# Performance work log

Measured on AMD Instinct MI355X. Metric: run time of the kernel, lower is better.

## Reference

```python
import jax, jax.numpy as jnp
from jax import lax
import numpy as np

VOCAB_SIZE = 510
N_LABELS = VOCAB_SIZE + 2  # 512; start_idx = N_LABELS-2, stop_idx = N_LABELS-1
BATCH = 128
SEQ_LEN = 256
NEG_INF = -10000.0  # matches torch fill value (finite, not -inf)


def setup_inputs() -> dict:
    key = jax.random.key(0)
    k_logits, k_lens, k_trans = jax.random.split(key, 3)
    logits = jax.random.normal(k_logits, (BATCH, SEQ_LEN, N_LABELS), dtype=jnp.float32)
    # lengths in [1, SEQ_LEN] so every sequence has at least one real step
    lens = jax.random.randint(k_lens, (BATCH,), 1, SEQ_LEN + 1, dtype=jnp.int64)
    # learned parameter: transitions[i, j] = score of transitioning j -> i
    transitions = jax.random.normal(k_trans, (N_LABELS, N_LABELS), dtype=jnp.float32)
    return {"logits": logits, "lens": lens, "transitions": transitions}


def reference(logits, lens, transitions):
    """CRF forward algorithm (log partition function). Returns norm: [batch]."""
    B, S, L = logits.shape
    start_idx = L - 2
    stop_idx = L - 1

    alpha0 = jnp.full((B, L), NEG_INF, dtype=logits.dtype).at[:, start_idx].set(0.0)

    def step(carry, logit_t):
        alpha, rem = carry  # alpha: [B, L], rem: [B]
        # scores[b, i, j] = transitions[i, j] + alpha[b, j] + logit_t[b, i]
        scores = transitions[None, :, :] + alpha[:, None, :] + logit_t[:, :, None]
        alpha_next = jax.nn.logsumexp(scores, axis=2)  # [B, L]
        mask = (rem > 0)[:, None]
        alpha = jnp.where(mask, alpha_next, alpha)
        return (alpha, rem - 1), None

    logits_t = jnp.swapaxes(logits, 0, 1)  # [S, B, L]
    (alpha, _), _ = lax.scan(step, (alpha0, lens), logits_t)

    alpha = alpha + transitions[stop_idx][None, :]
    norm = jax.nn.logsumexp(alpha, axis=1)  # [B]
    return norm
```

## Files before the change

kernel.cpp:

```cpp
#include <hip/hip_runtime.h>


typedef _Float16 h2 __attribute__((ext_vector_type(2)));

#define NB 128
#define NS 256
#define NL 512

#define SMEM_ELDS_BYTES (NL * 16 * 16)
#define SMEM_Y_OFF      SMEM_ELDS_BYTES
#define SMEM_RED_OFF    (SMEM_ELDS_BYTES + NL * 2)
#define SMEM_TOTAL      (SMEM_RED_OFF + 64)

__device__ __forceinline__ float dot2acc(unsigned int e, unsigned int y, float acc) {
#if __has_builtin(__builtin_amdgcn_fdot2)
    return __builtin_amdgcn_fdot2(__builtin_bit_cast(h2, e),
                                  __builtin_bit_cast(h2, y), acc, false);
#else
    h2 eh = __builtin_bit_cast(h2, e);
    h2 yh = __builtin_bit_cast(h2, y);
    return acc + (float)eh[0] * (float)yh[0] + (float)eh[1] * (float)yh[1];
#endif
}

__device__ __forceinline__ unsigned int pk2(float a, float b) {
    h2 h;
    h[0] = (_Float16)a;
    h[1] = (_Float16)b;
    return __builtin_bit_cast(unsigned int, h);
}

__global__ __launch_bounds__(512, 2) void crf_fwd_kernel(
    const float* __restrict__ logits,
    const int*   __restrict__ lens_raw,
    const float* __restrict__ trans,
    float* __restrict__ out)
{
    extern __shared__ char smem[];
    uint4*          e_lds = (uint4*)smem;
    unsigned short* y_sh  = (unsigned short*)(smem + SMEM_Y_OFF);
    float*          red   = (float*)(smem + SMEM_RED_OFF);

    const int b    = blockIdx.x;
    const int i    = threadIdx.x;
    const int lane = i & 63;
    const int wid  = i >> 6;
    const int swz  = i & 15;

    int len;
    {
        int s1 = lens_raw[1];
        len = (s1 == 0) ? lens_raw[2 * b] : lens_raw[b];
        len = min(max(len, 0), NS);
    }

    const float4* trow4 = (const float4*)(trans + (size_t)i * NL);

    float m = -3.4e38f;
    for (int c = 0; c < NL / 4; ++c) {
        float4 v = trow4[c];
        m = fmaxf(m, fmaxf(fmaxf(v.x, v.y), fmaxf(v.z, v.w)));
    }
    #pragma unroll
    for (int off = 32; off; off >>= 1) m = fmaxf(m, __shfl_xor(m, off));
    if (lane == 0) red[wid] = m;
    __syncthreads();
    float T = red[0];
    #pragma unroll
    for (int k = 1; k < 8; ++k) T = fmaxf(T, red[k]);
    __syncthreads();

    unsigned int Ereg[192];
    #pragma unroll
    for (int c = 0; c < 96; ++c) {
        float4 v = trow4[c];
        Ereg[2 * c]     = pk2(__expf(v.x - T), __expf(v.y - T));
        Ereg[2 * c + 1] = pk2(__expf(v.z - T), __expf(v.w - T));
    }
    #pragma unroll
    for (int c = 0; c < 16; ++c) {
        float4 a = trow4[96 + 2 * c];
        float4 d = trow4[97 + 2 * c];
        uint4 w;
        w.x = pk2(__expf(a.x - T), __expf(a.y - T));
        w.y = pk2(__expf(a.z - T), __expf(a.w - T));
        w.z = pk2(__expf(d.x - T), __expf(d.y - T));
        w.w = pk2(__expf(d.z - T), __expf(d.w - T));
        e_lds[i * 16 + (c ^ swz)] = w;
    }

    y_sh[i] = (i == NL - 2) ? (unsigned short)0x3C00u : (unsigned short)0u;
    float r = 0.0f;
    const float* lrow = logits + (size_t)b * NS * NL + i;
    __syncthreads();

    const uint4* y4   = (const uint4*)y_sh;
    const uint4* my_e = e_lds + i * 16;

    for (int t = 0; t < len; ++t) {
        float lg = lrow[(size_t)t * NL];
        float s0 = 0.f, s1 = 0.f, s2 = 0.f, s3 = 0.f;
        #pragma unroll
        for (int c = 0; c < 48; ++c) {
            uint4 yw = y4[c];
            s0 = dot2acc(Ereg[4 * c + 0], yw.x, s0);
            s1 = dot2acc(Ereg[4 * c + 1], yw.y, s1);
            s2 = dot2acc(Ereg[4 * c + 2], yw.z, s2);
            s3 = dot2acc(Ereg[4 * c + 3], yw.w, s3);
        }
        #pragma unroll
        for (int c = 0; c < 16; ++c) {
            uint4 ew = my_e[c ^ swz];
            uint4 yw = y4[48 + c];
            s0 = dot2acc(ew.x, yw.x, s0);
            s1 = dot2acc(ew.y, yw.y, s1);
            s2 = dot2acc(ew.z, yw.z, s2);
            s3 = dot2acc(ew.w, yw.w, s3);
        }
        float v = ((s0 + s1) + (s2 + s3)) * __expf(lg);

        float mv = v;
        #pragma unroll
        for (int off = 32; off; off >>= 1) mv = fmaxf(mv, __shfl_xor(mv, off));
        if (lane == 0) red[wid] = mv;
        __syncthreads();
        float cmax = red[0];
        #pragma unroll
        for (int k = 1; k < 8; ++k) cmax = fmaxf(cmax, red[k]);

        float yn = v * (1.0f / cmax);
        y_sh[i] = __builtin_bit_cast(unsigned short, (_Float16)yn);
        r += T + __logf(cmax);
        __syncthreads();
    }

    float yi;
    {
        _Float16 h = __builtin_bit_cast(_Float16, y_sh[i]);
        yi = (float)h;
    }
    float term = yi * __expf(trans[(size_t)(NL - 1) * NL + i] - T);
    #pragma unroll
    for (int off = 32; off; off >>= 1) term += __shfl_xor(term, off);
    if (lane == 0) red[wid] = term;
    __syncthreads();
    if (i == 0) {
        float tot = 0.f;
        #pragma unroll
        for (int k = 0; k < 8; ++k) tot += red[k];
        out[b] = r + T + __logf(tot);
    }
}

extern "C" void kernel_launch(void* const* d_in, const int* in_sizes, int n_in,
                              void* d_out, int out_size, void* d_ws, size_t ws_size,
                              hipStream_t stream) {
    const float* logits = (const float*)d_in[0];
    const int*   lens   = (const int*)d_in[1];
    const float* trans  = (const float*)d_in[2];
    float*       out    = (float*)d_out;

    hipFuncSetAttribute(reinterpret_cast<const void*>(crf_fwd_kernel),
                        hipFuncAttributeMaxDynamicSharedMemorySize, SMEM_TOTAL);

    crf_fwd_kernel<<<dim3(NB), dim3(512), SMEM_TOTAL, stream>>>(logits, lens, trans, out);
}
```

Before: 731.7 us.

## Split each transition row across two threads and hold exp-transitions fully in registers

Each label row is now handled by two threads of a 1024-thread block, each keeping 256 fp16 exp-transition values in 32 uint4 registers, so the LDS-resident portion of the matrix is dropped. The two partial dot products are combined with a lane shuffle. The logit for the next step is prefetched ahead of the recurrence. The goal is to halve the serial dot-product work per thread on each timestep and remove LDS traffic for transitions, at the cost of more waves per block and a 16-wave max reduction per step.

```diff
diff --git a/kernel.cpp b/kernel.cpp
--- a/kernel.cpp
+++ b/kernel.cpp
@@ -6,11 +6,6 @@
 #define NB 128
 #define NS 256
 #define NL 512
-
-#define SMEM_ELDS_BYTES (NL * 16 * 16)
-#define SMEM_Y_OFF      SMEM_ELDS_BYTES
-#define SMEM_RED_OFF    (SMEM_ELDS_BYTES + NL * 2)
-#define SMEM_TOTAL      (SMEM_RED_OFF + 64)
 
 __device__ __forceinline__ float dot2acc(unsigned int e, unsigned int y, float acc) {
 #if __has_builtin(__builtin_amdgcn_fdot2)
@@ -30,22 +25,27 @@
     return __builtin_bit_cast(unsigned int, h);
 }
 
-__global__ __launch_bounds__(512, 2) void crf_fwd_kernel(
+#define E_FOREACH(X) \
+    X(0) X(1) X(2) X(3) X(4) X(5) X(6) X(7) \
+    X(8) X(9) X(10) X(11) X(12) X(13) X(14) X(15) \
+    X(16) X(17) X(18) X(19) X(20) X(21) X(22) X(23) \
+    X(24) X(25) X(26) X(27) X(28) X(29) X(30) X(31)
+
+__global__ __launch_bounds__(1024, 4) void crf_fwd_kernel(
     const float* __restrict__ logits,
     const int*   __restrict__ lens_raw,
     const float* __restrict__ trans,
     float* __restrict__ out)
 {
-    extern __shared__ char smem[];
-    uint4*          e_lds = (uint4*)smem;
-    unsigned short* y_sh  = (unsigned short*)(smem + SMEM_Y_OFF);
-    float*          red   = (float*)(smem + SMEM_RED_OFF);
+    __shared__ unsigned short y_sh[NL];
+    __shared__ float red[16];
 
+    const int tid  = threadIdx.x;
+    const int row  = tid >> 1;
+    const int h    = tid & 1;
+    const int lane = tid & 63;
+    const int wid  = tid >> 6;
     const int b    = blockIdx.x;
-    const int i    = threadIdx.x;
-    const int lane = i & 63;
-    const int wid  = i >> 6;
-    const int swz  = i & 15;
 
     int len;
     {
@@ -54,10 +54,11 @@
         len = min(max(len, 0), NS);
     }
 
-    const float4* trow4 = (const float4*)(trans + (size_t)i * NL);
+    const float4* trow4 = (const float4*)(trans + (size_t)row * NL) + h * 64;
 
     float m = -3.4e38f;
-    for (int c = 0; c < NL / 4; ++c) {
+    #pragma unroll 8
+    for (int c = 0; c < 64; ++c) {
         float4 v = trow4[c];
         m = fmaxf(m, fmaxf(fmaxf(v.x, v.y), fmaxf(v.z, v.w)));
     }
@@ -67,87 +68,76 @@
     __syncthreads();
     float T = red[0];
     #pragma unroll
-    for (int k = 1; k < 8; ++k) T = fmaxf(T, red[k]);
+    for (int k = 1; k < 16; ++k) T = fmaxf(T, red[k]);
     __syncthreads();
 
-    unsigned int Ereg[192];
-    #pragma unroll
-    for (int c = 0; c < 96; ++c) {
-        float4 v = trow4[c];
-        Ereg[2 * c]     = pk2(__expf(v.x - T), __expf(v.y - T));
-        Ereg[2 * c + 1] = pk2(__expf(v.z - T), __expf(v.w - T));
-    }
-    #pragma unroll
-    for (int c = 0; c < 16; ++c) {
-        float4 a = trow4[96 + 2 * c];
-        float4 d = trow4[97 + 2 * c];
-        uint4 w;
-        w.x = pk2(__expf(a.x - T), __expf(a.y - T));
-        w.y = pk2(__expf(a.z - T), __expf(a.w - T));
-        w.z = pk2(__expf(d.x - T), __expf(d.y - T));
-        w.w = pk2(__expf(d.z - T), __expf(d.w - T));
-        e_lds[i * 16 + (c ^ swz)] = w;
-    }
+#define DECL_E(k) uint4 E##k;
+    E_FOREACH(DECL_E)
+#undef DECL_E
+#define LOAD_E(k) { \
+        float4 a_ = trow4[2 * (k)]; \
+        float4 d_ = trow4[2 * (k) + 1]; \
+        E##k.x = pk2(__expf(a_.x - T), __expf(a_.y - T)); \
+        E##k.y = pk2(__expf(a_.z - T), __expf(a_.w - T)); \
+        E##k.z = pk2(__expf(d_.x - T), __expf(d_.y - T)); \
+        E##k.w = pk2(__expf(d_.z - T), __expf(d_.w - T)); }
+    E_FOREACH(LOAD_E)
+#undef LOAD_E
 
-    y_sh[i] = (i == NL - 2) ? (unsigned short)0x3C00u : (unsigned short)0u;
+    if (h == 0) y_sh[row] = (row == NL - 2) ? (unsigned short)0x3C00u : (unsigned short)0u;
     float r = 0.0f;
-    const float* lrow = logits + (size_t)b * NS * NL + i;
+    const float* lrow = logits + (size_t)b * NS * NL + row;
     __syncthreads();
 
-    const uint4* y4   = (const uint4*)y_sh;
-    const uint4* my_e = e_lds + i * 16;
+    const uint4* y4 = (const uint4*)y_sh + h * 32;
 
+    float lg = lrow[0];
     for (int t = 0; t < len; ++t) {
-        float lg = lrow[(size_t)t * NL];
+        int tn = t + 1; if (tn >= len) tn = t;
+        float lg_next = lrow[(size_t)tn * NL];
+
         float s0 = 0.f, s1 = 0.f, s2 = 0.f, s3 = 0.f;
-        #pragma unroll
-        for (int c = 0; c < 48; ++c) {
-            uint4 yw = y4[c];
-            s0 = dot2acc(Ereg[4 * c + 0], yw.x, s0);
-            s1 = dot2acc(Ereg[4 * c + 1], yw.y, s1);
-            s2 = dot2acc(Ereg[4 * c + 2], yw.z, s2);
-            s3 = dot2acc(Ereg[4 * c + 3], yw.w, s3);
-        }
-        #pragma unroll
-        for (int c = 0; c < 16; ++c) {
-            uint4 ew = my_e[c ^ swz];
-            uint4 yw = y4[48 + c];
-            s0 = dot2acc(ew.x, yw.x, s0);
-            s1 = dot2acc(ew.y, yw.y, s1);
-            s2 = dot2acc(ew.z, yw.z, s2);
-            s3 = dot2acc(ew.w, yw.w, s3);
-        }
-        float v = ((s0 + s1) + (s2 + s3)) * __expf(lg);
+#define DOT_E(k) { \
+        uint4 yw = y4[(k)]; \
+        s0 = dot2acc(E##k.x, yw.x, s0); \
+        s1 = dot2acc(E##k.y, yw.y, s1); \
+        s2 = dot2acc(E##k.z, yw.z, s2); \
+        s3 = dot2acc(E##k.w, yw.w, s3); }
+        E_FOREACH(DOT_E)
+#undef DOT_E
+        float s = (s0 + s1) + (s2 + s3);
+        s += __shfl_xor(s, 1);
+        float v = s * __expf(lg);
 
         float mv = v;
         #pragma unroll
-        for (int off = 32; off; off >>= 1) mv = fmaxf(mv, __shfl_xor(mv, off));
+        for (int off = 32; off > 1; off >>= 1) mv = fmaxf(mv, __shfl_xor(mv, off));
         if (lane == 0) red[wid] = mv;
         __syncthreads();
         float cmax = red[0];
         #pragma unroll
-        for (int k = 1; k < 8; ++k) cmax = fmaxf(cmax, red[k]);
+        for (int k = 1; k < 16; ++k) cmax = fmaxf(cmax, red[k]);
 
-        float yn = v * (1.0f / cmax);
-        y_sh[i] = __builtin_bit_cast(unsigned short, (_Float16)yn);
+        if (h == 0)
+            y_sh[row] = __builtin_bit_cast(unsigned short, (_Float16)(v * (1.0f / cmax)));
         r += T + __logf(cmax);
+        lg = lg_next;
         __syncthreads();
     }
 
-    float yi;
-    {
-        _Float16 h = __builtin_bit_cast(_Float16, y_sh[i]);
-        yi = (float)h;
+    float term = 0.0f;
+    if (h == 0) {
+        _Float16 yh_ = __builtin_bit_cast(_Float16, y_sh[row]);
+        term = (float)yh_ * __expf(trans[(size_t)(NL - 1) * NL + row] - T);
     }
-    float term = yi * __expf(trans[(size_t)(NL - 1) * NL + i] - T);
     #pragma unroll
     for (int off = 32; off; off >>= 1) term += __shfl_xor(term, off);
     if (lane == 0) red[wid] = term;
     __syncthreads();
-    if (i == 0) {
+    if (tid == 0) {
         float tot = 0.f;
         #pragma unroll
-        for (int k = 0; k < 8; ++k) tot += red[k];
+        for (int k = 0; k < 16; ++k) tot += red[k];
         out[b] = r + T + __logf(tot);
     }
 }
@@ -160,8 +150,5 @@
     const float* trans  = (const float*)d_in[2];
     float*       out    = (float*)d_out;
 
-    hipFuncSetAttribute(reinterpret_cast<const void*>(crf_fwd_kernel),
-                        hipFuncAttributeMaxDynamicSharedMemorySize, SMEM_TOTAL);
-
-    crf_fwd_kernel<<<dim3(NB), dim3(512), SMEM_TOTAL, stream>>>(logits, lens, trans, out);
+    crf_fwd_kernel<<<dim3(NB), dim3(1024), 0, stream>>>(logits, lens, trans, out);
 }
```

After: 1.384 ms. 89.2% more time.
